# Optimization experiments

Measured on AMD Instinct MI355X. Metric: run time of the kernel, lower is better.

Reference implementation:

```python
import jax, jax.numpy as jnp
import numpy as np

X_SIZE, NUM_NEURONS, Z_SIZE = 2048, 4096, 64
D = X_SIZE + NUM_NEURONS + Z_SIZE  # 6208
TOPK, ZTOPK = 16, 8
EPS_TIE = 1e-9
RND = 0.5  # stand-in for random.random(); tie indicator t is 0 w.p. 1 for continuous inputs


def setup_inputs() -> dict:
    key = jax.random.key(0)
    k1, k2, k3, k4, k5 = jax.random.split(key, 5)
    x = jax.random.normal(k1, (X_SIZE,), dtype=jnp.float32)
    z = jax.random.normal(k2, (Z_SIZE,), dtype=jnp.float32)
    y_response = jax.random.uniform(k3, (NUM_NEURONS,), dtype=jnp.float32)
    neurons = jax.random.normal(k4, (D, D), dtype=jnp.float32)
    ages = 1.0 + 9.0 * jax.random.uniform(k5, (D,), dtype=jnp.float32)  # ages >= 1
    return {"x": x, "z": z, "y_response": y_response, "neurons": neurons, "ages": ages}


def _update_rows(neurons, ages, inpt, idx, vals):
    # Faithful to update_neuron_weights, including the (1,k)@(k,D) row-mix
    # that broadcasts the same mixed row to all k winner rows.
    a = ages[idx]                                   # (k,)
    upd = (vals / a)[:, None] * inpt[None, :]       # (k, D)
    mix = jnp.einsum('k,kd->d', (a - 1.0) / a, neurons[idx])  # (D,)
    new_rows = mix[None, :] + upd                   # (k, D)
    norm = jnp.sqrt(jnp.sum(new_rows * new_rows, axis=1, keepdims=True)) + 1e-12
    neurons = neurons.at[idx].set(new_rows / norm)
    ages = ages.at[idx].add(1.0)
    return neurons, ages


def reference(x, z, y_response, neurons, ages):
    # Steady-state path: num_neurons_init == max_num_neurons (> topk),
    # supervized_z = supervized_x = None, xtopk = None.
    x0, x1 = 0, X_SIZE
    y0, y1 = X_SIZE, X_SIZE + NUM_NEURONS
    z0 = X_SIZE + NUM_NEURONS

    inpt = jnp.concatenate([x, y_response, z])      # (D,)
    response = neurons @ inpt                       # (D,)
    final = jnp.zeros_like(response)

    # --- z path: top-(ztopk) winners, normalized against runner-up ---
    zvals, zidx = jax.lax.top_k(response[z0:], ZTOPK + 1)
    gz = z0 + zidx
    final = final.at[gz[:-1]].set((zvals[:-1] - zvals[-1]) / (zvals[0] - zvals[-1]))
    neurons, ages = _update_rows(neurons, ages, inpt, gz[:-1], zvals[:-1])

    # --- x path (xtopk None, unsupervised): normalize full x response ---
    rx = response[x0:x1]
    tx = jnp.where(jnp.all(rx == 0.0), 1.0, 0.0)
    xvals = rx / (jnp.max(rx) + EPS_TIE * tx * RND)
    final = final.at[x0:x1].set(xvals)
    xidx = jnp.arange(x0, x1)
    neurons, ages = _update_rows(neurons, ages, inpt, xidx[:-1], xvals[:-1])

    # --- y path: fully grown net -> topk winner-take-most branch ---
    yvals, yidx = jax.lax.top_k(response[y0:y1], TOPK + 1)
    gy = y0 + yidx
    ty = jnp.where(jnp.any(yvals[:-1] == yvals[-1]), 1.0, 0.0)
    final = final.at[gy[:-1]].set(
        (yvals[:-1] - yvals[-1]) / (yvals[0] - yvals[-1] + EPS_TIE * ty * RND))
    neurons, ages = _update_rows(neurons, ages, inpt, gy[:-1], yvals[:-1])

    z_response = final[z0:]
    return z_response, final, neurons, ages
```

## Files before the change

kernel.cpp:

```cpp
#include <hip/hip_runtime.h>
#include <math.h>

typedef float v4f __attribute__((ext_vector_type(4)));

#define XS 2048
#define NN 4096
#define ZS 64
#define DD 6208
#define D4 1552
#define Z0 (XS + NN)
#define TOPK 16
#define ZTOPK 8
#define EPS_TIE 1e-9f
#define RNDC 0.5f
#define NXUPD 2047

#define OUT_FINAL 64
#define OUT_NEUR  (64 + DD)
#define OUT_AGES  (OUT_NEUR + (size_t)DD * DD)

#define WS_RESP    0
#define WS_RESPP   DD
#define WS_INPT    (DD + 8192)
#define WS_MIXX    (WS_INPT + DD)
#define WS_MIXZ    (WS_MIXX + DD)
#define WS_MIXY    (WS_MIXZ + DD)
#define WS_SCAL    (WS_MIXY + DD)
#define WS_SCALPAD (WS_SCAL + 32)
#define WS_SELROW  (WS_SCALPAD + 448)
#define WS_SELC    (WS_SELROW + 24)
#define WS_SELW    (WS_SELC + 24)
#define WS_TOTAL   (WS_SELW + 32)


#define XBLKS 1024
#define CSPL  388
#define YZBLKS (DD - XS)
#define AUXBLKS 11

#define RBLKS 388
#define GBLKS 16

__device__ __forceinline__ v4f ld4(const float* p) { return *(const v4f*)p; }
__device__ __forceinline__ v4f v4z() { v4f v; v.x = v.y = v.z = v.w = 0.f; return v; }
__device__ __forceinline__ float dot4(v4f a, v4f b) {
  return fmaf(a.x, b.x, fmaf(a.y, b.y, fmaf(a.z, b.z, a.w * b.w)));
}
__device__ __forceinline__ v4f load_inpt(const float* x, const float* yr,
                                         const float* zv, int c) {
  int col = c * 4;
  if (col < XS) return ld4(x + col);
  if (col < Z0) return ld4(yr + (col - XS));
  return ld4(zv + (col - Z0));
}
__device__ __forceinline__ v4f wred4(v4f a) {
  #pragma unroll
  for (int m = 32; m >= 1; m >>= 1) {
    a.x += __shfl_xor(a.x, m); a.y += __shfl_xor(a.y, m);
    a.z += __shfl_xor(a.z, m); a.w += __shfl_xor(a.w, m);
  }
  return a;
}

__global__ __launch_bounds__(256, 4) void k_phase1(
    const float* __restrict__ x, const float* __restrict__ yr,
    const float* __restrict__ zv, const float* __restrict__ neurons,
    const float* __restrict__ ages, float* __restrict__ ws,
    float* __restrict__ out)
{
  const int t = threadIdx.x;
  const int b = blockIdx.x;
  float* outn = out + OUT_NEUR;

  if (b < XBLKS) {
    const int rg = b >> 2, cs = b & 3;
    const int row0 = rg * 8;
    const int cbase = cs * CSPL;
    const int c0 = cbase + t;
    const int c1 = cbase + 256 + t;
    const bool has1 = (t < CSPL - 256);

    v4f i0 = load_inpt(x, yr, zv, c0);
    v4f i1 = has1 ? load_inpt(x, yr, zv, c1) : v4z();
    if (b < 4) {
      ((v4f*)(ws + WS_INPT))[c0] = i0;
      if (has1) ((v4f*)(ws + WS_INPT))[c1] = i1;
    }

    float wr[8];
    #pragma unroll
    for (int r = 0; r < 8; ++r) {
      float a = ages[row0 + r];
      wr[r] = (row0 + r < NXUPD) ? (a - 1.f) / a : 0.f;
    }

    v4f a0[8], a1[8];
    #pragma unroll
    for (int r = 0; r < 8; ++r)
      a0[r] = ld4(neurons + (size_t)(row0 + r) * DD + 4 * c0);
    #pragma unroll
    for (int r = 0; r < 8; ++r)
      a1[r] = has1 ? ld4(neurons + (size_t)(row0 + r) * DD + 4 * c1) : v4z();

    float dot[8];
    v4f m0 = v4z(), m1 = v4z();
    #pragma unroll
    for (int r = 0; r < 8; ++r) {
      dot[r] = dot4(a0[r], i0) + dot4(a1[r], i1);
      m0 += wr[r] * a0[r];
      m1 += wr[r] * a1[r];
    }
    if (row0 + 7 >= NXUPD) {
      __builtin_nontemporal_store(a0[7], (v4f*)(outn + (size_t)2047 * DD + 4 * c0));
      if (has1)
        __builtin_nontemporal_store(a1[7], (v4f*)(outn + (size_t)2047 * DD + 4 * c1));
    }

    __shared__ float wred[4][8];
    const int lane = t & 63, wv = t >> 6;
    #pragma unroll
    for (int r = 0; r < 8; ++r) {
      float v = dot[r];
      #pragma unroll
      for (int m = 32; m >= 1; m >>= 1) v += __shfl_xor(v, m);
      if (lane == 0) wred[wv][r] = v;
    }
    __syncthreads();
    if (t < 8)
      ws[WS_RESPP + cs * 2048 + row0 + t] =
          wred[0][t] + wred[1][t] + wred[2][t] + wred[3][t];

    float* pm = outn + (size_t)rg * DD;
    *(v4f*)(pm + 4 * c0) = m0;
    if (has1) *(v4f*)(pm + 4 * c1) = m1;
  } else if (b < XBLKS + YZBLKS) {
    const int row = 2048 + (b - XBLKS);
    const float* rp = neurons + (size_t)row * DD;
    float* op = outn + (size_t)row * DD;

    v4f a[6], iv[6];
    #pragma unroll
    for (int k = 0; k < 6; ++k) a[k] = ld4(rp + 4 * (t + 256 * k));
    #pragma unroll
    for (int k = 0; k < 6; ++k) iv[k] = load_inpt(x, yr, zv, t + 256 * k);

    float dot = 0.f;
    #pragma unroll
    for (int k = 0; k < 6; ++k) {
      dot += dot4(a[k], iv[k]);
      __builtin_nontemporal_store(a[k], (v4f*)op + (t + 256 * k));
    }
    if (t < 16) {
      const int c = 1536 + t;
      v4f ae = ld4(rp + 4 * c);
      v4f ie = ld4(zv + (4 * c - Z0));
      dot += dot4(ae, ie);
      __builtin_nontemporal_store(ae, (v4f*)op + c);
    }
    __shared__ float red[4];
    const int lane = t & 63, wv = t >> 6;
    #pragma unroll
    for (int m = 32; m >= 1; m >>= 1) dot += __shfl_xor(dot, m);
    if (lane == 0) red[wv] = dot;
    __syncthreads();
    if (t == 0) ws[WS_RESP + row] = red[0] + red[1] + red[2] + red[3];
  } else {
    const int e = b - (XBLKS + YZBLKS);
    const int base = e * 1024;
    #pragma unroll
    for (int k = 0; k < 4; ++k) {
      int j = base + t + 256 * k;
      if (j < DD) {
        out[OUT_AGES + j] = ages[j] + ((j < NXUPD) ? 1.f : 0.f);
      } else {
        int f = j - DD;
        if (f < DD - XS) out[OUT_FINAL + XS + f] = 0.f;
      }
    }
  }
}

__global__ __launch_bounds__(1024) void k_phase2(
    const float* __restrict__ ages, float* __restrict__ ws, float* __restrict__ out)
{
  const int t = threadIdx.x;
  const int lane = t & 63, wv = t >> 6;
  __shared__ float s_xsum[XS];
  __shared__ float s_candv[16 * (TOPK + 1)];
  __shared__ int   s_candi[16 * (TOPK + 1)];
  __shared__ float s_zval[ZTOPK + 1];
  __shared__ int   s_zidx[ZTOPK + 1];
  __shared__ float s_yval[TOPK + 1];
  __shared__ int   s_yidx[TOPK + 1];
  __shared__ float s_red[16];
  __shared__ int   s_redi[16];
  __shared__ float s_denx, s_ty;

  float* resp = ws + WS_RESP;
  float* fin  = out + OUT_FINAL;
  float* oag  = out + OUT_AGES;

  if (t < 448) ws[WS_SCALPAD + t] = 0.f;

  {
    float v0 = 0.f, v1 = 0.f;
    #pragma unroll
    for (int cs = 0; cs < 4; ++cs) {
      v0 += ws[WS_RESPP + cs * 2048 + t];
      v1 += ws[WS_RESPP + cs * 2048 + t + 1024];
    }
    s_xsum[t] = v0; s_xsum[t + 1024] = v1;
    float lm = fmaxf(v0, v1);
    int nz = (v0 != 0.f) | (v1 != 0.f);
    #pragma unroll
    for (int m = 1; m < 64; m <<= 1) { lm = fmaxf(lm, __shfl_xor(lm, m)); nz |= __shfl_xor(nz, m); }
    if (lane == 0) { s_red[wv] = lm; s_redi[wv] = nz; }
  }

  {
    float v[4]; int id[4];
    #pragma unroll
    for (int q = 0; q < 4; ++q) { int i = (wv << 8) + (q << 6) + lane; id[q] = i; v[q] = resp[XS + i]; }
    for (int j = 0; j <= TOPK; ++j) {
      float bv = v[0]; int bi = id[0];
      #pragma unroll
      for (int q = 1; q < 4; ++q)
        if (v[q] > bv || (v[q] == bv && id[q] < bi)) { bv = v[q]; bi = id[q]; }
      #pragma unroll
      for (int m = 1; m < 64; m <<= 1) {
        float ov = __shfl_xor(bv, m); int oi = __shfl_xor(bi, m);
        if (ov > bv || (ov == bv && oi < bi)) { bv = ov; bi = oi; }
      }
      if (lane == 0) { s_candv[wv * (TOPK + 1) + j] = bv; s_candi[wv * (TOPK + 1) + j] = bi; }
      #pragma unroll
      for (int q = 0; q < 4; ++q) if (id[q] == bi) v[q] = -INFINITY;
    }
  }

  if (wv == 0) {
    float v = resp[Z0 + lane];
    for (int j = 0; j <= ZTOPK; ++j) {
      float bv = v; int bi = lane;
      #pragma unroll
      for (int m = 1; m < 64; m <<= 1) {
        float ov = __shfl_xor(bv, m); int oi = __shfl_xor(bi, m);
        if (ov > bv || (ov == bv && oi < bi)) { bv = ov; bi = oi; }
      }
      if (lane == 0) { s_zval[j] = bv; s_zidx[j] = bi; }
      if (lane == bi) v = -INFINITY;
    }
  }

  __syncthreads();

  if (t == 64) {
    float m2 = -INFINITY; int n2 = 0;
    for (int q = 0; q < 16; ++q) { m2 = fmaxf(m2, s_red[q]); n2 |= s_redi[q]; }
    float dx = m2 + EPS_TIE * (n2 ? 0.f : 1.f) * RNDC;
    s_denx = dx;
    ws[WS_SCAL + 7] = dx;
  }
  if (wv == 0) {
    float mv[5]; int mi[5];
    #pragma unroll
    for (int q = 0; q < 5; ++q) {
      int k = lane + (q << 6);
      if (k < 16 * (TOPK + 1)) { mv[q] = s_candv[k]; mi[q] = s_candi[k]; }
      else { mv[q] = -INFINITY; mi[q] = 0x7fffffff; }
    }
    for (int j = 0; j <= TOPK; ++j) {
      float bv = mv[0]; int bi = mi[0];
      #pragma unroll
      for (int q = 1; q < 5; ++q)
        if (mv[q] > bv || (mv[q] == bv && mi[q] < bi)) { bv = mv[q]; bi = mi[q]; }
      #pragma unroll
      for (int m = 1; m < 64; m <<= 1) {
        float ov = __shfl_xor(bv, m); int oi = __shfl_xor(bi, m);
        if (ov > bv || (ov == bv && oi < bi)) { bv = ov; bi = oi; }
      }
      if (lane == 0) { s_yval[j] = bv; s_yidx[j] = bi; }
      #pragma unroll
      for (int q = 0; q < 5; ++q) if (mi[q] == bi) mv[q] = -INFINITY;
    }
    if (lane == 0) {
      float ty = 0.f;
      for (int q = 0; q < TOPK; ++q) if (s_yval[q] == s_yval[TOPK]) ty = 1.f;
      s_ty = ty;
    }
  }
  __syncthreads();

  const float denx  = s_denx;
  fin[t]        = s_xsum[t] / denx;
  fin[t + 1024] = s_xsum[t + 1024] / denx;

  const float zlast = s_zval[ZTOPK];
  const float zden  = s_zval[0] - zlast;
  const float ylast = s_yval[TOPK];
  const float yden  = s_yval[0] - ylast + EPS_TIE * s_ty * RNDC;

  if (t < ZTOPK) {
    int zi = s_zidx[t];
    int row = Z0 + zi;
    fin[row] = (s_zval[t] - zlast) / zden;
    float a = ages[row];
    ((int*)(ws + WS_SELROW))[t] = row;
    ws[WS_SELC + t] = s_zval[t] / a;
    ws[WS_SELW + t] = (a - 1.f) / a;
    oag[row] = a + 1.f;
  } else if (t >= 32 && t < 32 + TOPK) {
    int k = t - 32;
    int row = XS + s_yidx[k];
    fin[row] = (s_yval[k] - ylast) / yden;
    float a = ages[row];
    ((int*)(ws + WS_SELROW))[ZTOPK + k] = row;
    ws[WS_SELC + ZTOPK + k] = s_yval[k] / a;
    ws[WS_SELW + ZTOPK + k] = (a - 1.f) / a;
    oag[row] = a + 1.f;
  } else if (t >= 128 && t < 192) {
    int i = t - 128;
    float v = 0.f;
    for (int k = 0; k < ZTOPK; ++k) if (s_zidx[k] == i) v = (s_zval[k] - zlast) / zden;
    out[i] = v;
  }
}

__global__ __launch_bounds__(256, 4) void k_phase3(
    const float* __restrict__ neurons, const float* __restrict__ outn,
    float* __restrict__ ws)
{
  const int b = blockIdx.x;
  const int t = threadIdx.x;

  if (b < RBLKS) {
    const int cb = 4 * b;
    const float* pr = outn + (size_t)t * DD + 4 * cb;
    v4f a0 = ld4(pr), a1 = ld4(pr + 4), a2 = ld4(pr + 8), a3 = ld4(pr + 12);
    a0 = wred4(a0); a1 = wred4(a1); a2 = wred4(a2); a3 = wred4(a3);
    __shared__ v4f sred[4][4];
    __shared__ float sp[4][3];
    if ((t & 63) == 0) {
      int w = t >> 6;
      sred[w][0] = a0; sred[w][1] = a1; sred[w][2] = a2; sred[w][3] = a3;
    }
    __syncthreads();
    if (t < 4) {
      v4f s = sred[0][t] + sred[1][t] + sred[2][t] + sred[3][t];
      *(v4f*)(ws + WS_MIXX + 4 * (cb + t)) = s;
      v4f ip = ld4(ws + WS_INPT + 4 * (cb + t));
      sp[t][0] = dot4(ip, ip);
      sp[t][1] = dot4(s, s);
      sp[t][2] = dot4(s, ip);
    }
    __syncthreads();
    if (t == 0) {
      const int slot = b & 63;
      #pragma unroll
      for (int k = 0; k < 3; ++k) {
        float p = sp[0][k] + sp[1][k] + sp[2][k] + sp[3][k];
        atomicAdd(ws + WS_SCALPAD + k * 64 + slot, p);
      }
    }
  } else {
    const int g = b - RBLKS;
    const int c = 97 * g + t;
    const int* selr = (const int*)(ws + WS_SELROW);
    float p0 = 0.f, p1 = 0.f, p2 = 0.f, p3 = 0.f;
    if (t < 97) {
      v4f mz = v4z(), my = v4z();
      #pragma unroll
      for (int k = 0; k < ZTOPK; ++k) {
        const int row = selr[k];
        const float w = ws[WS_SELW + k];
        mz += w * ld4(neurons + (size_t)row * DD + 4 * c);
      }
      #pragma unroll
      for (int k = ZTOPK; k < ZTOPK + TOPK; ++k) {
        const int row = selr[k];
        const float w = ws[WS_SELW + k];
        my += w * ld4(neurons + (size_t)row * DD + 4 * c);
      }
      *(v4f*)(ws + WS_MIXZ + 4 * c) = mz;
      *(v4f*)(ws + WS_MIXY + 4 * c) = my;
      v4f ip = ld4(ws + WS_INPT + 4 * c);
      p0 = dot4(mz, mz); p1 = dot4(mz, ip);
      p2 = dot4(my, my); p3 = dot4(my, ip);
    }
    #pragma unroll
    for (int m = 1; m < 64; m <<= 1) {
      p0 += __shfl_xor(p0, m); p1 += __shfl_xor(p1, m);
      p2 += __shfl_xor(p2, m); p3 += __shfl_xor(p3, m);
    }
    __shared__ float gr[4][4];
    if ((t & 63) == 0) {
      int w = t >> 6;
      gr[w][0] = p0; gr[w][1] = p1; gr[w][2] = p2; gr[w][3] = p3;
    }
    __syncthreads();
    if (t == 0) {
      const int slot = b & 63;
      #pragma unroll
      for (int k = 0; k < 4; ++k) {
        float p = gr[0][k] + gr[1][k] + gr[2][k] + gr[3][k];
        atomicAdd(ws + WS_SCALPAD + (3 + k) * 64 + slot, p);
      }
    }
  }
}

__global__ __launch_bounds__(256, 4) void k_phase4(
    const float* __restrict__ ages, const float* __restrict__ ws,
    float* __restrict__ outn)
{
  const int b = blockIdx.x;
  const int t = threadIdx.x;

  __shared__ float s_scal[7];
  if (t < 64) {
    #pragma unroll
    for (int k = 0; k < 7; ++k) {
      float v = ws[WS_SCALPAD + k * 64 + t];
      #pragma unroll
      for (int m = 1; m < 64; m <<= 1) v += __shfl_xor(v, m);
      if (t == 0) s_scal[k] = v;
    }
  }
  __syncthreads();

  const float sii = s_scal[0];
  int row; float c, smm, smi; const float* mix;
  if (b < NXUPD) {
    row = b;
    float a = ages[row];
    float rsum = ws[WS_RESPP + row] + ws[WS_RESPP + 2048 + row] +
                 ws[WS_RESPP + 4096 + row] + ws[WS_RESPP + 6144 + row];
    c = (rsum / ws[WS_SCAL + 7]) / a;
    mix = ws + WS_MIXX; smm = s_scal[1]; smi = s_scal[2];
  } else {
    int k = b - NXUPD;
    row = ((const int*)(ws + WS_SELROW))[k];
    c = ws[WS_SELC + k];
    if (k < ZTOPK) { mix = ws + WS_MIXZ; smm = s_scal[3]; smi = s_scal[4]; }
    else           { mix = ws + WS_MIXY; smm = s_scal[5]; smi = s_scal[6]; }
  }
  const float inv = 1.f / (sqrtf(fmaf(c, fmaf(c, sii, 2.f * smi), smm)) + 1e-12f);
  const float* inpt = ws + WS_INPT;
  float* dst = outn + (size_t)row * DD;
  #pragma unroll
  for (int k = 0; k < 6; ++k) {
    const int i = t + 256 * k;
    v4f m4 = ((const v4f*)(mix))[i];
    v4f i4 = ((const v4f*)(inpt))[i];
    v4f o = (m4 + c * i4) * inv;
    __builtin_nontemporal_store(o, (v4f*)dst + i);
  }
  if (t < 16) {
    const int i = 1536 + t;
    v4f m4 = ((const v4f*)(mix))[i];
    v4f i4 = ((const v4f*)(inpt))[i];
    v4f o = (m4 + c * i4) * inv;
    __builtin_nontemporal_store(o, (v4f*)dst + i);
  }
}

extern "C" void kernel_launch(void* const* d_in, const int* in_sizes, int n_in,
                              void* d_out, int out_size, void* d_ws, size_t ws_size,
                              hipStream_t stream)
{
  (void)in_sizes; (void)n_in; (void)out_size; (void)ws_size;
  const float* x    = (const float*)d_in[0];
  const float* zin  = (const float*)d_in[1];
  const float* yr   = (const float*)d_in[2];
  const float* neur = (const float*)d_in[3];
  const float* ages = (const float*)d_in[4];
  float* out = (float*)d_out;
  float* ws  = (float*)d_ws;

  k_phase1<<<XBLKS + YZBLKS + AUXBLKS, 256, 0, stream>>>(x, yr, zin, neur, ages, ws, out);
  k_phase2<<<1, 1024, 0, stream>>>(ages, ws, out);
  k_phase3<<<RBLKS + GBLKS, 256, 0, stream>>>(neur, out + OUT_NEUR, ws);
  k_phase4<<<NXUPD + ZTOPK + TOPK, 256, 0, stream>>>(ages, ws, out + OUT_NEUR);
}
```

Measured before the change: 317.6 us.

## Fuse four phase kernels into one cooperative persistent kernel with grid syncs

Replaces the four separate kernel launches with a single cooperative kernel of 1024 persistent blocks that loop over the virtual blocks of each phase, separated by grid-wide syncs. The single-block 1024-thread top-k/normalize phase is split across four 256-thread blocks (y top-k, x sum/max, z top-k, scratch zeroing), and the x response is materialized once instead of re-summed in the last phase. Phase 1 also streams rows one at a time instead of holding all 16 loads in registers. This removes launch gaps and the serial single-block phase, at the cost of grid sync overhead and a fixed grid of 1024 blocks that may underfill the memory-bound phases. A fallback to separate launches is used if the cooperative launch fails.

```diff
diff --git a/kernel.cpp b/kernel.cpp
--- a/kernel.cpp
+++ b/kernel.cpp
@@ -1,5 +1,8 @@
 #include <hip/hip_runtime.h>
+#include <hip/hip_cooperative_groups.h>
 #include <math.h>
+
+namespace cg = cooperative_groups;
 
 typedef float v4f __attribute__((ext_vector_type(4)));
 
@@ -37,9 +40,15 @@
 #define CSPL  388
 #define YZBLKS (DD - XS)
 #define AUXBLKS 11
+#define NVB_A (XBLKS + YZBLKS + AUXBLKS)
 
 #define RBLKS 388
 #define GBLKS 16
+#define NVB_C (RBLKS + GBLKS)
+
+#define NVB_D (NXUPD + ZTOPK + TOPK)
+
+#define GRIDN 1024
 
 __device__ __forceinline__ v4f ld4(const float* p) { return *(const v4f*)p; }
 __device__ __forceinline__ v4f v4z() { v4f v; v.x = v.y = v.z = v.w = 0.f; return v; }
@@ -62,18 +71,16 @@
   return a;
 }
 
-__global__ __launch_bounds__(256, 4) void k_phase1(
-    const float* __restrict__ x, const float* __restrict__ yr,
-    const float* __restrict__ zv, const float* __restrict__ neurons,
-    const float* __restrict__ ages, float* __restrict__ ws,
-    float* __restrict__ out)
-{
-  const int t = threadIdx.x;
-  const int b = blockIdx.x;
+
+__device__ __forceinline__ void bodyA(
+    int vb, int t, const float* x, const float* yr, const float* zv,
+    const float* neurons, const float* ages, float* ws, float* out,
+    float (*s_wred)[8], float* s_red4)
+{
   float* outn = out + OUT_NEUR;
 
-  if (b < XBLKS) {
-    const int rg = b >> 2, cs = b & 3;
+  if (vb < XBLKS) {
+    const int rg = vb >> 2, cs = vb & 3;
     const int row0 = rg * 8;
     const int cbase = cs * CSPL;
     const int c0 = cbase + t;
@@ -82,59 +89,49 @@
 
     v4f i0 = load_inpt(x, yr, zv, c0);
     v4f i1 = has1 ? load_inpt(x, yr, zv, c1) : v4z();
-    if (b < 4) {
+    if (vb < 4) {
       ((v4f*)(ws + WS_INPT))[c0] = i0;
       if (has1) ((v4f*)(ws + WS_INPT))[c1] = i1;
     }
 
-    float wr[8];
-    #pragma unroll
-    for (int r = 0; r < 8; ++r) {
-      float a = ages[row0 + r];
-      wr[r] = (row0 + r < NXUPD) ? (a - 1.f) / a : 0.f;
-    }
-
-    v4f a0[8], a1[8];
-    #pragma unroll
-    for (int r = 0; r < 8; ++r)
-      a0[r] = ld4(neurons + (size_t)(row0 + r) * DD + 4 * c0);
-    #pragma unroll
-    for (int r = 0; r < 8; ++r)
-      a1[r] = has1 ? ld4(neurons + (size_t)(row0 + r) * DD + 4 * c1) : v4z();
-
     float dot[8];
     v4f m0 = v4z(), m1 = v4z();
     #pragma unroll
     for (int r = 0; r < 8; ++r) {
-      dot[r] = dot4(a0[r], i0) + dot4(a1[r], i1);
-      m0 += wr[r] * a0[r];
-      m1 += wr[r] * a1[r];
-    }
-    if (row0 + 7 >= NXUPD) {
-      __builtin_nontemporal_store(a0[7], (v4f*)(outn + (size_t)2047 * DD + 4 * c0));
-      if (has1)
-        __builtin_nontemporal_store(a1[7], (v4f*)(outn + (size_t)2047 * DD + 4 * c1));
-    }
-
-    __shared__ float wred[4][8];
+      const int row = row0 + r;
+      const float* rp = neurons + (size_t)row * DD;
+      float a = ages[row];
+      float wr = (row < NXUPD) ? (a - 1.f) / a : 0.f;
+      v4f a0 = ld4(rp + 4 * c0);
+      v4f a1 = has1 ? ld4(rp + 4 * c1) : v4z();
+      dot[r] = dot4(a0, i0) + dot4(a1, i1);
+      m0 += wr * a0;
+      m1 += wr * a1;
+      if (row == 2047) {
+        __builtin_nontemporal_store(a0, (v4f*)(outn + (size_t)2047 * DD) + c0);
+        if (has1)
+          __builtin_nontemporal_store(a1, (v4f*)(outn + (size_t)2047 * DD) + c1);
+      }
+    }
+
     const int lane = t & 63, wv = t >> 6;
     #pragma unroll
     for (int r = 0; r < 8; ++r) {
       float v = dot[r];
       #pragma unroll
       for (int m = 32; m >= 1; m >>= 1) v += __shfl_xor(v, m);
-      if (lane == 0) wred[wv][r] = v;
+      if (lane == 0) s_wred[wv][r] = v;
     }
     __syncthreads();
     if (t < 8)
       ws[WS_RESPP + cs * 2048 + row0 + t] =
-          wred[0][t] + wred[1][t] + wred[2][t] + wred[3][t];
+          s_wred[0][t] + s_wred[1][t] + s_wred[2][t] + s_wred[3][t];
 
     float* pm = outn + (size_t)rg * DD;
     *(v4f*)(pm + 4 * c0) = m0;
     if (has1) *(v4f*)(pm + 4 * c1) = m1;
-  } else if (b < XBLKS + YZBLKS) {
-    const int row = 2048 + (b - XBLKS);
+  } else if (vb < XBLKS + YZBLKS) {
+    const int row = 2048 + (vb - XBLKS);
     const float* rp = neurons + (size_t)row * DD;
     float* op = outn + (size_t)row * DD;
 
@@ -157,15 +154,14 @@
       dot += dot4(ae, ie);
       __builtin_nontemporal_store(ae, (v4f*)op + c);
     }
-    __shared__ float red[4];
     const int lane = t & 63, wv = t >> 6;
     #pragma unroll
     for (int m = 32; m >= 1; m >>= 1) dot += __shfl_xor(dot, m);
-    if (lane == 0) red[wv] = dot;
-    __syncthreads();
-    if (t == 0) ws[WS_RESP + row] = red[0] + red[1] + red[2] + red[3];
+    if (lane == 0) s_red4[wv] = dot;
+    __syncthreads();
+    if (t == 0) ws[WS_RESP + row] = s_red4[0] + s_red4[1] + s_red4[2] + s_red4[3];
   } else {
-    const int e = b - (XBLKS + YZBLKS);
+    const int e = vb - (XBLKS + YZBLKS);
     const int base = e * 1024;
     #pragma unroll
     for (int k = 0; k < 4; ++k) {
@@ -180,189 +176,170 @@
   }
 }
 
-__global__ __launch_bounds__(1024) void k_phase2(
-    const float* __restrict__ ages, float* __restrict__ ws, float* __restrict__ out)
-{
-  const int t = threadIdx.x;
+__device__ __forceinline__ void bodyB(
+    int rb, int t, const float* ages, float* ws, float* out,
+    float* smf, int* smi)
+{
   const int lane = t & 63, wv = t >> 6;
-  __shared__ float s_xsum[XS];
-  __shared__ float s_candv[16 * (TOPK + 1)];
-  __shared__ int   s_candi[16 * (TOPK + 1)];
-  __shared__ float s_zval[ZTOPK + 1];
-  __shared__ int   s_zidx[ZTOPK + 1];
-  __shared__ float s_yval[TOPK + 1];
-  __shared__ int   s_yidx[TOPK + 1];
-  __shared__ float s_red[16];
-  __shared__ int   s_redi[16];
-  __shared__ float s_denx, s_ty;
-
-  float* resp = ws + WS_RESP;
-  float* fin  = out + OUT_FINAL;
-  float* oag  = out + OUT_AGES;
-
-  if (t < 448) ws[WS_SCALPAD + t] = 0.f;
-
-  {
-    float v0 = 0.f, v1 = 0.f;
-    #pragma unroll
-    for (int cs = 0; cs < 4; ++cs) {
-      v0 += ws[WS_RESPP + cs * 2048 + t];
-      v1 += ws[WS_RESPP + cs * 2048 + t + 1024];
-    }
-    s_xsum[t] = v0; s_xsum[t + 1024] = v1;
-    float lm = fmaxf(v0, v1);
-    int nz = (v0 != 0.f) | (v1 != 0.f);
-    #pragma unroll
-    for (int m = 1; m < 64; m <<= 1) { lm = fmaxf(lm, __shfl_xor(lm, m)); nz |= __shfl_xor(nz, m); }
-    if (lane == 0) { s_red[wv] = lm; s_redi[wv] = nz; }
-  }
-
-  {
-    float v[4]; int id[4];
-    #pragma unroll
-    for (int q = 0; q < 4; ++q) { int i = (wv << 8) + (q << 6) + lane; id[q] = i; v[q] = resp[XS + i]; }
+  float* fin = out + OUT_FINAL;
+  float* oag = out + OUT_AGES;
+
+  if (rb == 0) {
+    float v[16]; int id[16];
+    #pragma unroll
+    for (int q = 0; q < 16; ++q) {
+      int i = (wv << 10) + (q << 6) + lane;
+      id[q] = i; v[q] = ws[WS_RESP + XS + i];
+    }
     for (int j = 0; j <= TOPK; ++j) {
       float bv = v[0]; int bi = id[0];
       #pragma unroll
-      for (int q = 1; q < 4; ++q)
+      for (int q = 1; q < 16; ++q)
         if (v[q] > bv || (v[q] == bv && id[q] < bi)) { bv = v[q]; bi = id[q]; }
       #pragma unroll
       for (int m = 1; m < 64; m <<= 1) {
         float ov = __shfl_xor(bv, m); int oi = __shfl_xor(bi, m);
         if (ov > bv || (ov == bv && oi < bi)) { bv = ov; bi = oi; }
       }
-      if (lane == 0) { s_candv[wv * (TOPK + 1) + j] = bv; s_candi[wv * (TOPK + 1) + j] = bi; }
-      #pragma unroll
-      for (int q = 0; q < 4; ++q) if (id[q] == bi) v[q] = -INFINITY;
-    }
-  }
-
-  if (wv == 0) {
-    float v = resp[Z0 + lane];
-    for (int j = 0; j <= ZTOPK; ++j) {
-      float bv = v; int bi = lane;
-      #pragma unroll
-      for (int m = 1; m < 64; m <<= 1) {
-        float ov = __shfl_xor(bv, m); int oi = __shfl_xor(bi, m);
-        if (ov > bv || (ov == bv && oi < bi)) { bv = ov; bi = oi; }
-      }
-      if (lane == 0) { s_zval[j] = bv; s_zidx[j] = bi; }
-      if (lane == bi) v = -INFINITY;
-    }
-  }
-
-  __syncthreads();
-
-  if (t == 64) {
-    float m2 = -INFINITY; int n2 = 0;
-    for (int q = 0; q < 16; ++q) { m2 = fmaxf(m2, s_red[q]); n2 |= s_redi[q]; }
-    float dx = m2 + EPS_TIE * (n2 ? 0.f : 1.f) * RNDC;
-    s_denx = dx;
-    ws[WS_SCAL + 7] = dx;
-  }
-  if (wv == 0) {
-    float mv[5]; int mi[5];
-    #pragma unroll
-    for (int q = 0; q < 5; ++q) {
-      int k = lane + (q << 6);
-      if (k < 16 * (TOPK + 1)) { mv[q] = s_candv[k]; mi[q] = s_candi[k]; }
-      else { mv[q] = -INFINITY; mi[q] = 0x7fffffff; }
-    }
-    for (int j = 0; j <= TOPK; ++j) {
-      float bv = mv[0]; int bi = mi[0];
-      #pragma unroll
-      for (int q = 1; q < 5; ++q)
-        if (mv[q] > bv || (mv[q] == bv && mi[q] < bi)) { bv = mv[q]; bi = mi[q]; }
-      #pragma unroll
-      for (int m = 1; m < 64; m <<= 1) {
-        float ov = __shfl_xor(bv, m); int oi = __shfl_xor(bi, m);
-        if (ov > bv || (ov == bv && oi < bi)) { bv = ov; bi = oi; }
-      }
-      if (lane == 0) { s_yval[j] = bv; s_yidx[j] = bi; }
-      #pragma unroll
-      for (int q = 0; q < 5; ++q) if (mi[q] == bi) mv[q] = -INFINITY;
-    }
-    if (lane == 0) {
+      if (lane == 0) { smf[wv * 17 + j] = bv; smi[wv * 17 + j] = bi; }
+      #pragma unroll
+      for (int q = 0; q < 16; ++q) if (id[q] == bi) v[q] = -INFINITY;
+    }
+    __syncthreads();
+    if (wv == 0) {
+      float mv0 = smf[lane];            int mi0 = smi[lane];
+      float mv1 = (lane < 4) ? smf[64 + lane] : -INFINITY;
+      int   mi1 = (lane < 4) ? smi[64 + lane] : 0x7fffffff;
+      for (int j = 0; j <= TOPK; ++j) {
+        float bv = mv0; int bi = mi0;
+        if (mv1 > bv || (mv1 == bv && mi1 < bi)) { bv = mv1; bi = mi1; }
+        #pragma unroll
+        for (int m = 1; m < 64; m <<= 1) {
+          float ov = __shfl_xor(bv, m); int oi = __shfl_xor(bi, m);
+          if (ov > bv || (ov == bv && oi < bi)) { bv = ov; bi = oi; }
+        }
+        if (lane == 0) { smf[68 + j] = bv; smi[68 + j] = bi; }
+        if (mi0 == bi) mv0 = -INFINITY;
+        if (mi1 == bi) mv1 = -INFINITY;
+      }
+    }
+    __syncthreads();
+    if (t == 0) {
+      float ylast = smf[68 + TOPK];
       float ty = 0.f;
-      for (int q = 0; q < TOPK; ++q) if (s_yval[q] == s_yval[TOPK]) ty = 1.f;
-      s_ty = ty;
-    }
-  }
-  __syncthreads();
-
-  const float denx  = s_denx;
-  fin[t]        = s_xsum[t] / denx;
-  fin[t + 1024] = s_xsum[t + 1024] / denx;
-
-  const float zlast = s_zval[ZTOPK];
-  const float zden  = s_zval[0] - zlast;
-  const float ylast = s_yval[TOPK];
-  const float yden  = s_yval[0] - ylast + EPS_TIE * s_ty * RNDC;
-
-  if (t < ZTOPK) {
-    int zi = s_zidx[t];
-    int row = Z0 + zi;
-    fin[row] = (s_zval[t] - zlast) / zden;
-    float a = ages[row];
-    ((int*)(ws + WS_SELROW))[t] = row;
-    ws[WS_SELC + t] = s_zval[t] / a;
-    ws[WS_SELW + t] = (a - 1.f) / a;
-    oag[row] = a + 1.f;
-  } else if (t >= 32 && t < 32 + TOPK) {
-    int k = t - 32;
-    int row = XS + s_yidx[k];
-    fin[row] = (s_yval[k] - ylast) / yden;
-    float a = ages[row];
-    ((int*)(ws + WS_SELROW))[ZTOPK + k] = row;
-    ws[WS_SELC + ZTOPK + k] = s_yval[k] / a;
-    ws[WS_SELW + ZTOPK + k] = (a - 1.f) / a;
-    oag[row] = a + 1.f;
-  } else if (t >= 128 && t < 192) {
-    int i = t - 128;
-    float v = 0.f;
-    for (int k = 0; k < ZTOPK; ++k) if (s_zidx[k] == i) v = (s_zval[k] - zlast) / zden;
-    out[i] = v;
-  }
-}
-
-__global__ __launch_bounds__(256, 4) void k_phase3(
-    const float* __restrict__ neurons, const float* __restrict__ outn,
-    float* __restrict__ ws)
-{
-  const int b = blockIdx.x;
-  const int t = threadIdx.x;
-
-  if (b < RBLKS) {
-    const int cb = 4 * b;
+      for (int q = 0; q < TOPK; ++q) if (smf[68 + q] == ylast) ty = 1.f;
+      smf[85] = ty;
+    }
+    __syncthreads();
+    if (t < TOPK) {
+      float ylast = smf[68 + TOPK];
+      float yden = smf[68] - ylast + EPS_TIE * smf[85] * RNDC;
+      int row = XS + smi[68 + t];
+      fin[row] = (smf[68 + t] - ylast) / yden;
+      float a = ages[row];
+      ((int*)(ws + WS_SELROW))[ZTOPK + t] = row;
+      ws[WS_SELC + ZTOPK + t] = smf[68 + t] / a;
+      ws[WS_SELW + ZTOPK + t] = (a - 1.f) / a;
+      oag[row] = a + 1.f;
+    }
+  } else if (rb == 1) {
+    float s[8]; float lm = -INFINITY; int nz = 0;
+    #pragma unroll
+    for (int k = 0; k < 8; ++k) {
+      int i = t + 256 * k;
+      float v = ws[WS_RESPP + i] + ws[WS_RESPP + 2048 + i] +
+                ws[WS_RESPP + 4096 + i] + ws[WS_RESPP + 6144 + i];
+      s[k] = v;
+      ws[WS_RESP + i] = v;
+      lm = fmaxf(lm, v); nz |= (v != 0.f);
+    }
+    #pragma unroll
+    for (int m = 1; m < 64; m <<= 1) { lm = fmaxf(lm, __shfl_xor(lm, m)); nz |= __shfl_xor(nz, m); }
+    if (lane == 0) { smf[wv] = lm; smi[wv] = nz; }
+    __syncthreads();
+    if (t == 0) {
+      float m2 = fmaxf(fmaxf(smf[0], smf[1]), fmaxf(smf[2], smf[3]));
+      int n2 = smi[0] | smi[1] | smi[2] | smi[3];
+      float dx = m2 + EPS_TIE * (n2 ? 0.f : 1.f) * RNDC;
+      smf[4] = dx; ws[WS_SCAL + 7] = dx;
+    }
+    __syncthreads();
+    float dx = smf[4];
+    #pragma unroll
+    for (int k = 0; k < 8; ++k) fin[t + 256 * k] = s[k] / dx;
+  } else if (rb == 2) {
+    if (wv == 0) {
+      float v = ws[WS_RESP + Z0 + lane];
+      for (int j = 0; j <= ZTOPK; ++j) {
+        float bv = v; int bi = lane;
+        #pragma unroll
+        for (int m = 1; m < 64; m <<= 1) {
+          float ov = __shfl_xor(bv, m); int oi = __shfl_xor(bi, m);
+          if (ov > bv || (ov == bv && oi < bi)) { bv = ov; bi = oi; }
+        }
+        if (lane == 0) { smf[j] = bv; smi[j] = bi; }
+        if (lane == bi) v = -INFINITY;
+      }
+    }
+    __syncthreads();
+    float zlast = smf[ZTOPK], zden = smf[0] - zlast;
+    if (t < ZTOPK) {
+      int row = Z0 + smi[t];
+      fin[row] = (smf[t] - zlast) / zden;
+      float a = ages[row];
+      ((int*)(ws + WS_SELROW))[t] = row;
+      ws[WS_SELC + t] = smf[t] / a;
+      ws[WS_SELW + t] = (a - 1.f) / a;
+      oag[row] = a + 1.f;
+    }
+    if (t >= 128 && t < 192) {
+      int i = t - 128;
+      float v = 0.f;
+      for (int k = 0; k < ZTOPK; ++k) if (smi[k] == i) v = (smf[k] - zlast) / zden;
+      out[i] = v;
+    }
+  } else if (rb == 3) {
+    ws[WS_SCALPAD + t] = 0.f;
+    if (t < 192) ws[WS_SCALPAD + 256 + t] = 0.f;
+  }
+}
+
+__device__ __forceinline__ void bodyC(
+    int vb, int t, const float* neurons, const float* outn, float* ws,
+    float* smf)
+{
+  const int lane = t & 63, wv = t >> 6;
+  if (vb < RBLKS) {
+    const int cb = 4 * vb;
     const float* pr = outn + (size_t)t * DD + 4 * cb;
     v4f a0 = ld4(pr), a1 = ld4(pr + 4), a2 = ld4(pr + 8), a3 = ld4(pr + 12);
     a0 = wred4(a0); a1 = wred4(a1); a2 = wred4(a2); a3 = wred4(a3);
-    __shared__ v4f sred[4][4];
-    __shared__ float sp[4][3];
-    if ((t & 63) == 0) {
-      int w = t >> 6;
-      sred[w][0] = a0; sred[w][1] = a1; sred[w][2] = a2; sred[w][3] = a3;
+    v4f* sred = (v4f*)smf;
+    float* sp = smf + 64;
+    if (lane == 0) {
+      sred[wv * 4 + 0] = a0; sred[wv * 4 + 1] = a1;
+      sred[wv * 4 + 2] = a2; sred[wv * 4 + 3] = a3;
     }
     __syncthreads();
     if (t < 4) {
-      v4f s = sred[0][t] + sred[1][t] + sred[2][t] + sred[3][t];
+      v4f s = sred[t] + sred[4 + t] + sred[8 + t] + sred[12 + t];
       *(v4f*)(ws + WS_MIXX + 4 * (cb + t)) = s;
       v4f ip = ld4(ws + WS_INPT + 4 * (cb + t));
-      sp[t][0] = dot4(ip, ip);
-      sp[t][1] = dot4(s, s);
-      sp[t][2] = dot4(s, ip);
+      sp[t * 3 + 0] = dot4(ip, ip);
+      sp[t * 3 + 1] = dot4(s, s);
+      sp[t * 3 + 2] = dot4(s, ip);
     }
     __syncthreads();
     if (t == 0) {
-      const int slot = b & 63;
+      const int slot = vb & 63;
       #pragma unroll
       for (int k = 0; k < 3; ++k) {
-        float p = sp[0][k] + sp[1][k] + sp[2][k] + sp[3][k];
+        float p = sp[k] + sp[3 + k] + sp[6 + k] + sp[9 + k];
         atomicAdd(ws + WS_SCALPAD + k * 64 + slot, p);
       }
     }
   } else {
-    const int g = b - RBLKS;
+    const int g = vb - RBLKS;
     const int c = 97 * g + t;
     const int* selr = (const int*)(ws + WS_SELROW);
     float p0 = 0.f, p1 = 0.f, p2 = 0.f, p3 = 0.f;
@@ -391,59 +368,42 @@
       p0 += __shfl_xor(p0, m); p1 += __shfl_xor(p1, m);
       p2 += __shfl_xor(p2, m); p3 += __shfl_xor(p3, m);
     }
-    __shared__ float gr[4][4];
-    if ((t & 63) == 0) {
-      int w = t >> 6;
-      gr[w][0] = p0; gr[w][1] = p1; gr[w][2] = p2; gr[w][3] = p3;
+    float* gr = smf;
+    if (lane == 0) {
+      gr[wv * 4 + 0] = p0; gr[wv * 4 + 1] = p1;
+      gr[wv * 4 + 2] = p2; gr[wv * 4 + 3] = p3;
     }
     __syncthreads();
     if (t == 0) {
-      const int slot = b & 63;
+      const int slot = vb & 63;
       #pragma unroll
       for (int k = 0; k < 4; ++k) {
-        float p = gr[0][k] + gr[1][k] + gr[2][k] + gr[3][k];
+        float p = gr[k] + gr[4 + k] + gr[8 + k] + gr[12 + k];
         atomicAdd(ws + WS_SCALPAD + (3 + k) * 64 + slot, p);
       }
     }
   }
 }
 
-__global__ __launch_bounds__(256, 4) void k_phase4(
-    const float* __restrict__ ages, const float* __restrict__ ws,
-    float* __restrict__ outn)
-{
-  const int b = blockIdx.x;
-  const int t = threadIdx.x;
-
-  __shared__ float s_scal[7];
-  if (t < 64) {
-    #pragma unroll
-    for (int k = 0; k < 7; ++k) {
-      float v = ws[WS_SCALPAD + k * 64 + t];
-      #pragma unroll
-      for (int m = 1; m < 64; m <<= 1) v += __shfl_xor(v, m);
-      if (t == 0) s_scal[k] = v;
-    }
-  }
-  __syncthreads();
-
+__device__ __forceinline__ void bodyD(
+    int vb, int t, const float* ages, const float* ws, float* outn,
+    const float* s_scal)
+{
   const float sii = s_scal[0];
-  int row; float c, smm, smi; const float* mix;
-  if (b < NXUPD) {
-    row = b;
+  int row; float c, smm, smi_; const float* mix;
+  if (vb < NXUPD) {
+    row = vb;
     float a = ages[row];
-    float rsum = ws[WS_RESPP + row] + ws[WS_RESPP + 2048 + row] +
-                 ws[WS_RESPP + 4096 + row] + ws[WS_RESPP + 6144 + row];
-    c = (rsum / ws[WS_SCAL + 7]) / a;
-    mix = ws + WS_MIXX; smm = s_scal[1]; smi = s_scal[2];
+    c = (ws[WS_RESP + row] / ws[WS_SCAL + 7]) / a;
+    mix = ws + WS_MIXX; smm = s_scal[1]; smi_ = s_scal[2];
   } else {
-    int k = b - NXUPD;
+    int k = vb - NXUPD;
     row = ((const int*)(ws + WS_SELROW))[k];
     c = ws[WS_SELC + k];
-    if (k < ZTOPK) { mix = ws + WS_MIXZ; smm = s_scal[3]; smi = s_scal[4]; }
-    else           { mix = ws + WS_MIXY; smm = s_scal[5]; smi = s_scal[6]; }
-  }
-  const float inv = 1.f / (sqrtf(fmaf(c, fmaf(c, sii, 2.f * smi), smm)) + 1e-12f);
+    if (k < ZTOPK) { mix = ws + WS_MIXZ; smm = s_scal[3]; smi_ = s_scal[4]; }
+    else           { mix = ws + WS_MIXY; smm = s_scal[5]; smi_ = s_scal[6]; }
+  }
+  const float inv = 1.f / (sqrtf(fmaf(c, fmaf(c, sii, 2.f * smi_), smm)) + 1e-12f);
   const float* inpt = ws + WS_INPT;
   float* dst = outn + (size_t)row * DD;
   #pragma unroll
@@ -463,6 +423,101 @@
   }
 }
 
+__global__ __launch_bounds__(256, 4) void k_fused(
+    const float* __restrict__ x, const float* __restrict__ yr,
+    const float* __restrict__ zv, const float* __restrict__ neurons,
+    const float* __restrict__ ages, float* __restrict__ ws,
+    float* __restrict__ out)
+{
+  cg::grid_group grid = cg::this_grid();
+  const int t = threadIdx.x;
+  const int rb = blockIdx.x;
+
+  __shared__ float s_wred[4][8];
+  __shared__ float s_red4[4];
+  __shared__ float smf[96];
+  __shared__ int   smi[96];
+  __shared__ float s_scal[7];
+
+  for (int vb = rb; vb < NVB_A; vb += GRIDN) {
+    bodyA(vb, t, x, yr, zv, neurons, ages, ws, out, s_wred, s_red4);
+    __syncthreads();
+  }
+  __threadfence();
+  grid.sync();
+  __threadfence();
+
+  if (rb < 4) bodyB(rb, t, ages, ws, out, smf, smi);
+  __threadfence();
+  grid.sync();
+  __threadfence();
+
+  if (rb < NVB_C) bodyC(rb, t, neurons, out + OUT_NEUR, ws, smf);
+  __threadfence();
+  grid.sync();
+  __threadfence();
+
+  if (t < 64) {
+    #pragma unroll
+    for (int k = 0; k < 7; ++k) {
+      float v = ws[WS_SCALPAD + k * 64 + t];
+      #pragma unroll
+      for (int m = 1; m < 64; m <<= 1) v += __shfl_xor(v, m);
+      if (t == 0) s_scal[k] = v;
+    }
+  }
+  __syncthreads();
+  for (int vb = rb; vb < NVB_D; vb += GRIDN) {
+    bodyD(vb, t, ages, ws, out + OUT_NEUR, s_scal);
+  }
+}
+
+__global__ __launch_bounds__(256, 4) void k_pA(
+    const float* __restrict__ x, const float* __restrict__ yr,
+    const float* __restrict__ zv, const float* __restrict__ neurons,
+    const float* __restrict__ ages, float* __restrict__ ws,
+    float* __restrict__ out)
+{
+  __shared__ float s_wred[4][8];
+  __shared__ float s_red4[4];
+  bodyA(blockIdx.x, threadIdx.x, x, yr, zv, neurons, ages, ws, out, s_wred, s_red4);
+}
+
+__global__ __launch_bounds__(256) void k_pB(
+    const float* __restrict__ ages, float* __restrict__ ws, float* __restrict__ out)
+{
+  __shared__ float smf[96];
+  __shared__ int   smi[96];
+  bodyB(blockIdx.x, threadIdx.x, ages, ws, out, smf, smi);
+}
+
+__global__ __launch_bounds__(256, 4) void k_pC(
+    const float* __restrict__ neurons, const float* __restrict__ outn,
+    float* __restrict__ ws)
+{
+  __shared__ float smf[96];
+  bodyC(blockIdx.x, threadIdx.x, neurons, outn, ws, smf);
+}
+
+__global__ __launch_bounds__(256, 4) void k_pD(
+    const float* __restrict__ ages, const float* __restrict__ ws,
+    float* __restrict__ outn)
+{
+  const int t = threadIdx.x;
+  __shared__ float s_scal[7];
+  if (t < 64) {
+    #pragma unroll
+    for (int k = 0; k < 7; ++k) {
+      float v = ws[WS_SCALPAD + k * 64 + t];
+      #pragma unroll
+      for (int m = 1; m < 64; m <<= 1) v += __shfl_xor(v, m);
+      if (t == 0) s_scal[k] = v;
+    }
+  }
+  __syncthreads();
+  bodyD(blockIdx.x, t, ages, ws, outn, s_scal);
+}
+
 extern "C" void kernel_launch(void* const* d_in, const int* in_sizes, int n_in,
                               void* d_out, int out_size, void* d_ws, size_t ws_size,
                               hipStream_t stream)
@@ -476,8 +531,16 @@
   float* out = (float*)d_out;
   float* ws  = (float*)d_ws;
 
-  k_phase1<<<XBLKS + YZBLKS + AUXBLKS, 256, 0, stream>>>(x, yr, zin, neur, ages, ws, out);
-  k_phase2<<<1, 1024, 0, stream>>>(ages, ws, out);
-  k_phase3<<<RBLKS + GBLKS, 256, 0, stream>>>(neur, out + OUT_NEUR, ws);
-  k_phase4<<<NXUPD + ZTOPK + TOPK, 256, 0, stream>>>(ages, ws, out + OUT_NEUR);
-}
+  void* args[] = { (void*)&x, (void*)&yr, (void*)&zin, (void*)&neur,
+                   (void*)&ages, (void*)&ws, (void*)&out };
+  hipError_t e = hipLaunchCooperativeKernel((const void*)k_fused,
+                                            dim3(GRIDN), dim3(256),
+                                            args, 0, stream);
+  if (e != hipSuccess) {
+    (void)hipGetLastError();
+    k_pA<<<NVB_A, 256, 0, stream>>>(x, yr, zin, neur, ages, ws, out);
+    k_pB<<<4, 256, 0, stream>>>(ages, ws, out);
+    k_pC<<<NVB_C, 256, 0, stream>>>(neur, out + OUT_NEUR, ws);
+    k_pD<<<NVB_D, 256, 0, stream>>>(ages, ws, out + OUT_NEUR);
+  }
+}
```

Result: slower. 1.116 ms (+251.3%).
